# Performance work log

Hardware: AMD Instinct MI355X
Metric: run time of the kernel (lower is better)

The kernel has to match this reference:

```python
import jax, jax.numpy as jnp
import numpy as np

D_MODEL = 512
N_HEADS = 8
N_KV_HEADS = 2
HEAD_DIM = 64
PITCH_VOCAB = 128


def setup_inputs() -> dict:
    key = jax.random.key(0)
    ks = jax.random.split(key, 6)
    B, T, P = 2, 256, 12
    s = lambda fan_in: 1.0 / np.sqrt(fan_in)
    hidden_states = jax.random.normal(ks[0], (B, T, P, D_MODEL), dtype=jnp.float32)
    Wq = jax.random.normal(ks[1], (D_MODEL, N_HEADS * HEAD_DIM), dtype=jnp.float32) * s(D_MODEL)
    Wk = jax.random.normal(ks[2], (D_MODEL, N_KV_HEADS * HEAD_DIM), dtype=jnp.float32) * s(D_MODEL)
    Wv = jax.random.normal(ks[3], (D_MODEL, N_KV_HEADS * HEAD_DIM), dtype=jnp.float32) * s(D_MODEL)
    Wo = jax.random.normal(ks[4], (N_HEADS * HEAD_DIM, D_MODEL), dtype=jnp.float32) * s(N_HEADS * HEAD_DIM)
    pitch_table = jax.random.normal(ks[5], (PITCH_VOCAB, HEAD_DIM), dtype=jnp.float32)
    return {"hidden_states": hidden_states, "Wq": Wq, "Wk": Wk, "Wv": Wv, "Wo": Wo, "pitch_table": pitch_table}


def reference(hidden_states, Wq, Wk, Wv, Wo, pitch_table):
    B, T, P, C = hidden_states.shape
    H, Hkv, d = N_HEADS, N_KV_HEADS, HEAD_DIM
    rep = H // Hkv

    q = (hidden_states @ Wq).reshape(B, T, P, H, d)
    k = (hidden_states @ Wk).reshape(B, T, P, Hkv, d)
    v = (hidden_states @ Wv).reshape(B, T, P, Hkv, d)

    # GQA repeat_kv: (B,T,P,Hkv,d) -> (B,T,P,H,d)
    k = jnp.repeat(k, rep, axis=3)
    v = jnp.repeat(v, rep, axis=3)

    # additive pitch bias on q and k
    pitch_emb = pitch_table[jnp.arange(P)]  # (P, d)
    bias = pitch_emb[None, None, :, None, :]
    q = q + bias
    k = k + bias

    # flatten (T,P) -> S and move heads forward: (B,H,S,d)
    S = T * P
    q = q.transpose(0, 3, 1, 2, 4).reshape(B, H, S, d)
    k = k.transpose(0, 3, 1, 2, 4).reshape(B, H, S, d)
    v = v.transpose(0, 3, 1, 2, 4).reshape(B, H, S, d)

    scale = 1.0 / jnp.sqrt(jnp.asarray(d, dtype=q.dtype))
    attn = jax.nn.softmax(jnp.einsum('bhqd,bhkd->bhqk', q, k) * scale, axis=-1)
    out = jnp.einsum('bhqk,bhkd->bhqd', attn, v)  # (B,H,S,d)

    out = out.reshape(B, H, T, P, d).transpose(0, 2, 3, 1, 4).reshape(B, T, P, H * d)
    return out @ Wo
```

## Files before the change

kernel.cpp:

```cpp
#include <hip/hip_runtime.h>
#include <hip/hip_fp16.h>

#define B_   2
#define T_   256
#define P_   12
#define C_   512
#define H_   8
#define HKV_ 2
#define D_   64
#define S_   (T_ * P_)
#define M_   (B_ * S_)
#define NQKV 768
#define KSPLIT 2
#define KHALF (S_ / KSPLIT)

typedef _Float16 half8_t __attribute__((ext_vector_type(8)));
typedef _Float16 half4_t __attribute__((ext_vector_type(4)));
typedef _Float16 half2_t __attribute__((ext_vector_type(2)));
typedef float    float4_t __attribute__((ext_vector_type(4)));

#if __has_builtin(__builtin_amdgcn_exp2f)
#define EXP2(x) __builtin_amdgcn_exp2f(x)
#else
#define EXP2(x) __expf((x) * 0.69314718f)
#endif

static __device__ inline half2_t pack_h2(float a, float b) {
#if __has_builtin(__builtin_amdgcn_cvt_pkrtz)
    return __builtin_bit_cast(half2_t, __builtin_amdgcn_cvt_pkrtz(a, b));
#else
    half2_t r; r[0] = (_Float16)a; r[1] = (_Float16)b; return r;
#endif
}

#define SOFT_SHIFT 20.0f
#define SOFT_CLAMP 35.5f
#define QSCALE (0.125f * 1.44269504f)

__global__ __launch_bounds__(256) void prep_kernel(
    const float* __restrict__ hs,
    const float* __restrict__ Wq, const float* __restrict__ Wk,
    const float* __restrict__ Wv, const float* __restrict__ Wo,
    _Float16* __restrict__ hs16,
    _Float16* __restrict__ wcatT,
    _Float16* __restrict__ woT)
{
    const int blk = blockIdx.x;
    const int tid = threadIdx.x;

    if (blk < 160) {
        __shared__ __attribute__((aligned(16))) _Float16 Ts[64][72];
        const float* src; int srcN, col0; _Float16* dst; int n0, k0;
        if (blk < 96) {
            int nt = blk / 8, kt = blk % 8;
            n0 = nt * 64; k0 = kt * 64; dst = wcatT;
            if (n0 < 512)      { src = Wq; srcN = 512; col0 = n0; }
            else if (n0 < 640) { src = Wk; srcN = 128; col0 = n0 - 512; }
            else               { src = Wv; srcN = 128; col0 = n0 - 640; }
        } else {
            int t = blk - 96;
            int nt = t / 8, kt = t % 8;
            n0 = nt * 64; k0 = kt * 64; dst = woT;
            src = Wo; srcN = 512; col0 = n0;
        }
#pragma unroll
        for (int i = 0; i < 4; ++i) {
            int row = i * 16 + (tid >> 4);
            int cg  = tid & 15;
            float4_t v = *(const float4_t*)(src + (size_t)(k0 + row) * srcN + col0 + cg * 4);
            Ts[cg * 4 + 0][row] = (_Float16)v[0];
            Ts[cg * 4 + 1][row] = (_Float16)v[1];
            Ts[cg * 4 + 2][row] = (_Float16)v[2];
            Ts[cg * 4 + 3][row] = (_Float16)v[3];
        }
        __syncthreads();
#pragma unroll
        for (int i = 0; i < 2; ++i) {
            int seg = i * 256 + tid;
            int row = seg >> 3, s = seg & 7;
            *(half8_t*)(dst + (size_t)(n0 + row) * 512 + k0 + s * 8) =
                *(const half8_t*)&Ts[row][s * 8];
        }
    } else {
        int base = (blk - 160) * 4096;
#pragma unroll
        for (int i = 0; i < 16; ++i) {
            int f4 = base + i * 256 + tid;
            float4_t v = *(const float4_t*)(hs + (size_t)f4 * 4);
            half4_t hv;
            hv[0] = (_Float16)v[0]; hv[1] = (_Float16)v[1];
            hv[2] = (_Float16)v[2]; hv[3] = (_Float16)v[3];
            *(half4_t*)(hs16 + (size_t)f4 * 4) = hv;
        }
    }
}

__global__ __launch_bounds__(256) void qkv_kernel(
    const _Float16* __restrict__ A,
    const _Float16* __restrict__ WT,
    const float* __restrict__ pitch,
    _Float16* __restrict__ qb,
    _Float16* __restrict__ kb,
    _Float16* __restrict__ vb)
{
    const int m0   = blockIdx.x * 64;
    const int n0   = blockIdx.y * 128;
    const int tid  = threadIdx.x;
    const int wv   = tid >> 6;
    const int lane = tid & 63;
    const int ln   = lane & 15;
    const int quad = lane >> 4;
    const int wm   = (wv & 1) * 32;
    const int wn   = (wv >> 1) * 64;

    __shared__ __attribute__((aligned(16))) _Float16 As[64][72];
    __shared__ __attribute__((aligned(16))) _Float16 Bs[128][72];

    float4_t acc[2][4];
#pragma unroll
    for (int ms = 0; ms < 2; ++ms)
#pragma unroll
        for (int nt = 0; nt < 4; ++nt) acc[ms][nt] = (float4_t){0.f, 0.f, 0.f, 0.f};

    const int srow = tid >> 3;
    const int ss   = tid & 7;

    half8_t ar[2], br[4];
#pragma unroll
    for (int i = 0; i < 2; ++i)
        ar[i] = *(const half8_t*)&A[(size_t)(m0 + i * 32 + srow) * 512 + ss * 8];
#pragma unroll
    for (int i = 0; i < 4; ++i)
        br[i] = *(const half8_t*)&WT[(size_t)(n0 + i * 32 + srow) * 512 + ss * 8];

    for (int k0 = 0; k0 < 512; k0 += 64) {
        __syncthreads();
#pragma unroll
        for (int i = 0; i < 2; ++i) *(half8_t*)&As[i * 32 + srow][ss * 8] = ar[i];
#pragma unroll
        for (int i = 0; i < 4; ++i) *(half8_t*)&Bs[i * 32 + srow][ss * 8] = br[i];
        __syncthreads();

        if (k0 + 64 < 512) {
#pragma unroll
            for (int i = 0; i < 2; ++i)
                ar[i] = *(const half8_t*)&A[(size_t)(m0 + i * 32 + srow) * 512 + k0 + 64 + ss * 8];
#pragma unroll
            for (int i = 0; i < 4; ++i)
                br[i] = *(const half8_t*)&WT[(size_t)(n0 + i * 32 + srow) * 512 + k0 + 64 + ss * 8];
        }

#pragma unroll
        for (int ks = 0; ks < 2; ++ks) {
            half8_t af[2];
#pragma unroll
            for (int ms = 0; ms < 2; ++ms)
                af[ms] = *(const half8_t*)&As[wm + ms * 16 + ln][ks * 32 + quad * 8];
#pragma unroll
            for (int nt = 0; nt < 4; ++nt) {
                half8_t bf = *(const half8_t*)&Bs[wn + nt * 16 + ln][ks * 32 + quad * 8];
#pragma unroll
                for (int ms = 0; ms < 2; ++ms)
                    acc[ms][nt] = __builtin_amdgcn_mfma_f32_16x16x32_f16(af[ms], bf, acc[ms][nt], 0, 0, 0);
            }
        }
    }

    const int region = (n0 < 512) ? 0 : (n0 < 640 ? 1 : 2);
#pragma unroll
    for (int ms = 0; ms < 2; ++ms) {
#pragma unroll
        for (int nt = 0; nt < 4; ++nt) {
            int n = n0 + wn + nt * 16 + ln;
#pragma unroll
            for (int r = 0; r < 4; ++r) {
                int m = m0 + wm + ms * 16 + quad * 4 + r;
                int b = m / S_;
                int s = m - b * S_;
                int p = s % P_;
                float v = acc[ms][nt][r];
                if (region == 0) {
                    int h = n >> 6, dd = n & 63;
                    v = (v + pitch[p * 64 + dd]) * QSCALE;
                    qb[(((size_t)(b * H_ + h)) * S_ + s) * 64 + dd] = (_Float16)v;
                } else if (region == 1) {
                    int nn = n - 512, h = nn >> 6, dd = nn & 63;
                    v = v + pitch[p * 64 + dd];
                    kb[(((size_t)(b * HKV_ + h)) * S_ + s) * 64 + dd] = (_Float16)v;
                } else {
                    int nn = n - 640, h = nn >> 6, dd = nn & 63;
                    vb[(((size_t)(b * HKV_ + h)) * 64 + dd) * S_ + s] = (_Float16)v;
                }
            }
        }
    }
}

__global__ __launch_bounds__(256) void attn_kernel(
    const _Float16* __restrict__ qbuf,
    const _Float16* __restrict__ kbuf,
    const _Float16* __restrict__ vtb,
    _Float16* __restrict__ opA,
    _Float16* __restrict__ opB,
    float* __restrict__ lpA,
    float* __restrict__ lpB)
{
    const int qblk = blockIdx.x;
    const int bh   = blockIdx.y;
    const int kz   = blockIdx.z;
    const int bb   = bh >> 3;
    const int h    = bh & 7;
    const int hkv  = h >> 2;
    const int tid  = threadIdx.x;
    const int w    = tid >> 6;
    const int lane = tid & 63;
    const int ln   = lane & 15;
    const int quad = lane >> 4;

    _Float16* op = kz ? opB : opA;
    float*    lp = kz ? lpB : lpA;

    const _Float16* Q  = qbuf + ((size_t)(bb * H_ + h)) * S_ * 64;
    const _Float16* K  = kbuf + ((size_t)(bb * HKV_ + hkv)) * S_ * 64;
    const _Float16* Vt = vtb  + ((size_t)(bb * HKV_ + hkv)) * 64 * S_;

    __shared__ __attribute__((aligned(16))) _Float16 Ks[64][80];
    __shared__ __attribute__((aligned(16))) _Float16 VT[64][80];
    __shared__ __attribute__((aligned(16))) _Float16 Ps[4][32][40];

    const int qbase = qblk * 64 + (w & 1) * 32;
    const int kk0   = (w >> 1) * 32;
    const int ktlo  = kz * KHALF;

    half8_t qfrag[2][2];
#pragma unroll
    for (int sub = 0; sub < 2; ++sub)
#pragma unroll
        for (int ks = 0; ks < 2; ++ks)
            qfrag[sub][ks] = *(const half8_t*)&Q[(size_t)(qbase + sub * 16 + ln) * 64 + ks * 32 + quad * 8];

    float4_t o[2][4];
#pragma unroll
    for (int sub = 0; sub < 2; ++sub)
#pragma unroll
        for (int nt = 0; nt < 4; ++nt) o[sub][nt] = (float4_t){0.f, 0.f, 0.f, 0.f};
    float lr[2][4] = {{0.f,0.f,0.f,0.f},{0.f,0.f,0.f,0.f}};

    const int j0 = tid >> 3, s0 = tid & 7;
    const int j1 = j0 + 32;
    const int r0 = ((j0 & 1) << 4) | ((j0 >> 5) << 5) | ((j0 >> 1) & 15);
    const int r1 = ((j1 & 1) << 4) | ((j1 >> 5) << 5) | ((j1 >> 1) & 15);

    half8_t kr0, kr1, vr0, vr1;
    kr0 = *(const half8_t*)&K[(size_t)(ktlo + j0) * 64 + s0 * 8];
    kr1 = *(const half8_t*)&K[(size_t)(ktlo + j1) * 64 + s0 * 8];
    vr0 = *(const half8_t*)&Vt[(size_t)j0 * S_ + ktlo + s0 * 8];
    vr1 = *(const half8_t*)&Vt[(size_t)j1 * S_ + ktlo + s0 * 8];

    for (int kt = ktlo; kt < ktlo + KHALF; kt += 64) {
        __syncthreads();
        *(half8_t*)&Ks[r0][s0 * 8] = kr0;
        *(half8_t*)&Ks[r1][s0 * 8] = kr1;
        *(half8_t*)&VT[j0][s0 * 8] = vr0;
        *(half8_t*)&VT[j1][s0 * 8] = vr1;
        __syncthreads();

        if (kt + 64 < ktlo + KHALF) {
            kr0 = *(const half8_t*)&K[(size_t)(kt + 64 + j0) * 64 + s0 * 8];
            kr1 = *(const half8_t*)&K[(size_t)(kt + 64 + j1) * 64 + s0 * 8];
            vr0 = *(const half8_t*)&Vt[(size_t)j0 * S_ + kt + 64 + s0 * 8];
            vr1 = *(const half8_t*)&Vt[(size_t)j1 * S_ + kt + 64 + s0 * 8];
        }

        float4_t sf[2][2];
#pragma unroll
        for (int c = 0; c < 2; ++c) {
            sf[c][0] = (float4_t){0.f, 0.f, 0.f, 0.f};
            sf[c][1] = (float4_t){0.f, 0.f, 0.f, 0.f};
#pragma unroll
            for (int ks = 0; ks < 2; ++ks) {
                half8_t kf = *(const half8_t*)&Ks[kk0 + c * 16 + ln][ks * 32 + quad * 8];
                sf[c][0] = __builtin_amdgcn_mfma_f32_16x16x32_f16(qfrag[0][ks], kf, sf[c][0], 0, 0, 0);
                sf[c][1] = __builtin_amdgcn_mfma_f32_16x16x32_f16(qfrag[1][ks], kf, sf[c][1], 0, 0, 0);
            }
        }

#pragma unroll
        for (int sub = 0; sub < 2; ++sub) {
#pragma unroll
            for (int r = 0; r < 4; ++r) {
                float p0 = EXP2(fminf(sf[0][sub][r], SOFT_CLAMP) - SOFT_SHIFT);
                float p1 = EXP2(fminf(sf[1][sub][r], SOFT_CLAMP) - SOFT_SHIFT);
                lr[sub][r] += p0 + p1;
                *(half2_t*)&Ps[w][sub * 16 + quad * 4 + r][2 * ln] = pack_h2(p0, p1);
            }
        }

        half8_t pf0 = *(const half8_t*)&Ps[w][ln][quad * 8];
        half8_t pf1 = *(const half8_t*)&Ps[w][16 + ln][quad * 8];
#pragma unroll
        for (int nt = 0; nt < 4; ++nt) {
            half8_t vf = *(const half8_t*)&VT[nt * 16 + ln][kk0 + quad * 8];
            o[0][nt] = __builtin_amdgcn_mfma_f32_16x16x32_f16(pf0, vf, o[0][nt], 0, 0, 0);
            o[1][nt] = __builtin_amdgcn_mfma_f32_16x16x32_f16(pf1, vf, o[1][nt], 0, 0, 0);
        }
    }

    __syncthreads();
    if (w >= 2) {
        float* od = (w == 2) ? (float*)&Ks[0][0] : (float*)&VT[0][0];
#pragma unroll
        for (int sub = 0; sub < 2; ++sub)
#pragma unroll
            for (int nt = 0; nt < 4; ++nt)
                *(float4_t*)&od[lane * 32 + (sub * 4 + nt) * 4] = o[sub][nt];
        float* ld = (float*)&Ps[0][0][0] + (w - 2) * 512;
#pragma unroll
        for (int sub = 0; sub < 2; ++sub)
#pragma unroll
            for (int r = 0; r < 4; ++r)
                ld[lane * 8 + sub * 4 + r] = lr[sub][r];
    }
    __syncthreads();
    if (w < 2) {
        const float* os = (w == 0) ? (const float*)&Ks[0][0] : (const float*)&VT[0][0];
        const float* ls = (const float*)&Ps[0][0][0] + w * 512;
#pragma unroll
        for (int sub = 0; sub < 2; ++sub) {
#pragma unroll
            for (int r = 0; r < 4; ++r) {
                float l = lr[sub][r] + ls[lane * 8 + sub * 4 + r];
                l += __shfl_xor(l, 1);
                l += __shfl_xor(l, 2);
                l += __shfl_xor(l, 4);
                l += __shfl_xor(l, 8);
                float inv = 1.0f / l;
                int qg = qbase + sub * 16 + quad * 4 + r;
                size_t base = ((size_t)(bb * S_ + qg)) * 512 + h * 64;
#pragma unroll
                for (int nt = 0; nt < 4; ++nt) {
                    float vsum = o[sub][nt][r] + os[lane * 32 + (sub * 4 + nt) * 4 + r];
                    op[base + nt * 16 + ln] = (_Float16)(vsum * inv);
                }
                if (ln == 0)
                    lp[(size_t)(bb * H_ + h) * S_ + qg] = l;
            }
        }
    }
}

__global__ __launch_bounds__(256) void combine_kernel(
    _Float16* __restrict__ opA,
    const _Float16* __restrict__ opB,
    const float* __restrict__ lpA,
    const float* __restrict__ lpB)
{
    int i = blockIdx.x * 256 + threadIdx.x;
    int base = i * 8;
    int bs  = base >> 9;
    int col = base & 511;
    int h   = col >> 6;
    int b   = (bs >= S_) ? 1 : 0;
    int q   = bs - b * S_;
    size_t row = (size_t)(b * H_ + h) * S_ + q;
    float la = lpA[row], lb = lpB[row];
    float s  = la + lb;
    float wa = la / s, wb = lb / s;
    half8_t a8 = *(const half8_t*)(opA + (size_t)base);
    half8_t b8 = *(const half8_t*)(opB + (size_t)base);
    half8_t o8;
#pragma unroll
    for (int j = 0; j < 8; ++j)
        o8[j] = (_Float16)((float)a8[j] * wa + (float)b8[j] * wb);
    *(half8_t*)(opA + (size_t)base) = o8;
}

__global__ __launch_bounds__(256) void proj_out_kernel(
    const _Float16* __restrict__ A,
    const _Float16* __restrict__ WT,
    float* __restrict__ outp)
{
    const int m0   = blockIdx.x * 64;
    const int n0   = blockIdx.y * 128;
    const int tid  = threadIdx.x;
    const int wv   = tid >> 6;
    const int lane = tid & 63;
    const int ln   = lane & 15;
    const int quad = lane >> 4;
    const int wm   = (wv & 1) * 32;
    const int wn   = (wv >> 1) * 64;

    __shared__ __attribute__((aligned(16))) _Float16 As[64][72];
    __shared__ __attribute__((aligned(16))) _Float16 Bs[128][72];

    float4_t acc[2][4];
#pragma unroll
    for (int ms = 0; ms < 2; ++ms)
#pragma unroll
        for (int nt = 0; nt < 4; ++nt) acc[ms][nt] = (float4_t){0.f, 0.f, 0.f, 0.f};

    const int srow = tid >> 3;
    const int ss   = tid & 7;

    half8_t ar[2], br[4];
#pragma unroll
    for (int i = 0; i < 2; ++i)
        ar[i] = *(const half8_t*)&A[(size_t)(m0 + i * 32 + srow) * 512 + ss * 8];
#pragma unroll
    for (int i = 0; i < 4; ++i)
        br[i] = *(const half8_t*)&WT[(size_t)(n0 + i * 32 + srow) * 512 + ss * 8];

    for (int k0 = 0; k0 < 512; k0 += 64) {
        __syncthreads();
#pragma unroll
        for (int i = 0; i < 2; ++i) *(half8_t*)&As[i * 32 + srow][ss * 8] = ar[i];
#pragma unroll
        for (int i = 0; i < 4; ++i) *(half8_t*)&Bs[i * 32 + srow][ss * 8] = br[i];
        __syncthreads();

        if (k0 + 64 < 512) {
#pragma unroll
            for (int i = 0; i < 2; ++i)
                ar[i] = *(const half8_t*)&A[(size_t)(m0 + i * 32 + srow) * 512 + k0 + 64 + ss * 8];
#pragma unroll
            for (int i = 0; i < 4; ++i)
                br[i] = *(const half8_t*)&WT[(size_t)(n0 + i * 32 + srow) * 512 + k0 + 64 + ss * 8];
        }

#pragma unroll
        for (int ks = 0; ks < 2; ++ks) {
            half8_t af[2];
#pragma unroll
            for (int ms = 0; ms < 2; ++ms)
                af[ms] = *(const half8_t*)&As[wm + ms * 16 + ln][ks * 32 + quad * 8];
#pragma unroll
            for (int nt = 0; nt < 4; ++nt) {
                half8_t bf = *(const half8_t*)&Bs[wn + nt * 16 + ln][ks * 32 + quad * 8];
#pragma unroll
                for (int ms = 0; ms < 2; ++ms)
                    acc[ms][nt] = __builtin_amdgcn_mfma_f32_16x16x32_f16(af[ms], bf, acc[ms][nt], 0, 0, 0);
            }
        }
    }

#pragma unroll
    for (int ms = 0; ms < 2; ++ms) {
#pragma unroll
        for (int nt = 0; nt < 4; ++nt) {
            int n = n0 + wn + nt * 16 + ln;
#pragma unroll
            for (int r = 0; r < 4; ++r) {
                int m = m0 + wm + ms * 16 + quad * 4 + r;
                outp[(size_t)m * 512 + n] = acc[ms][nt][r];
            }
        }
    }
}

extern "C" void kernel_launch(void* const* d_in, const int* in_sizes, int n_in,
                              void* d_out, int out_size, void* d_ws, size_t ws_size,
                              hipStream_t stream) {
    const float* hs    = (const float*)d_in[0];
    const float* Wq    = (const float*)d_in[1];
    const float* Wk    = (const float*)d_in[2];
    const float* Wv    = (const float*)d_in[3];
    const float* Wo    = (const float*)d_in[4];
    const float* pitch = (const float*)d_in[5];
    float* out = (float*)d_out;

    _Float16* hs16  = (_Float16*)d_ws;
    _Float16* opA   = hs16;
    _Float16* q_buf = hs16 + (size_t)M_ * 512;
    _Float16* k_buf = q_buf + (size_t)B_ * H_ * S_ * 64;
    _Float16* v_buf = k_buf + (size_t)B_ * HKV_ * S_ * 64;
    _Float16* wcatT = v_buf + (size_t)B_ * HKV_ * S_ * 64;
    _Float16* woT   = wcatT + (size_t)NQKV * 512;
    _Float16* opB   = woT   + (size_t)512 * 512;
    float*    lpA   = (float*)(opB + (size_t)M_ * 512);
    float*    lpB   = lpA + (size_t)B_ * H_ * S_;

    prep_kernel<<<352, 256, 0, stream>>>(hs, Wq, Wk, Wv, Wo, hs16, wcatT, woT);
    qkv_kernel<<<dim3(M_ / 64, NQKV / 128), 256, 0, stream>>>(hs16, wcatT, pitch, q_buf, k_buf, v_buf);
    attn_kernel<<<dim3(S_ / 64, B_ * H_, KSPLIT), 256, 0, stream>>>(q_buf, k_buf, v_buf, opA, opB, lpA, lpB);
    combine_kernel<<<(M_ * 512 / 8) / 256, 256, 0, stream>>>(opA, opB, lpA, lpB);
    proj_out_kernel<<<dim3(M_ / 64, 4), 256, 0, stream>>>(opA, woT, out);
}
```

Measured before the change: 181.5 us.

## Enlarge attention tile to 128 queries with 512 threads and fold softmax shift

The attention kernel now runs 8 waves per block covering 128 query rows, so each K/V tile staged in shared memory is reused by twice as many queries. Each thread loads only one K and one V vector per tile. The softmax shift is folded into the MFMA accumulator initial value, and the row sum now uses a packed fp16 dot2 on the packed probabilities. Row-sum reductions move before the cross-wave combine, and the scratch buffers are laid out as an LDS union. The risks are fewer blocks in flight, heavier register and LDS use per block, and fp16 rounding in the row sum.

```diff
diff --git a/kernel.cpp b/kernel.cpp
--- a/kernel.cpp
+++ b/kernel.cpp
@@ -17,6 +17,7 @@
 typedef _Float16 half8_t __attribute__((ext_vector_type(8)));
 typedef _Float16 half4_t __attribute__((ext_vector_type(4)));
 typedef _Float16 half2_t __attribute__((ext_vector_type(2)));
+typedef __fp16   raw2_t  __attribute__((ext_vector_type(2)));
 typedef float    float4_t __attribute__((ext_vector_type(4)));
 
 #if __has_builtin(__builtin_amdgcn_exp2f)
@@ -25,16 +26,8 @@
 #define EXP2(x) __expf((x) * 0.69314718f)
 #endif
 
-static __device__ inline half2_t pack_h2(float a, float b) {
-#if __has_builtin(__builtin_amdgcn_cvt_pkrtz)
-    return __builtin_bit_cast(half2_t, __builtin_amdgcn_cvt_pkrtz(a, b));
-#else
-    half2_t r; r[0] = (_Float16)a; r[1] = (_Float16)b; return r;
-#endif
-}
-
 #define SOFT_SHIFT 20.0f
-#define SOFT_CLAMP 35.5f
+#define SOFT_CLAMP2 15.5f
 #define QSCALE (0.125f * 1.44269504f)
 
 __global__ __launch_bounds__(256) void prep_kernel(
@@ -196,7 +189,7 @@
     }
 }
 
-__global__ __launch_bounds__(256) void attn_kernel(
+__global__ __launch_bounds__(512) void attn_kernel(
     const _Float16* __restrict__ qbuf,
     const _Float16* __restrict__ kbuf,
     const _Float16* __restrict__ vtb,
@@ -224,12 +217,17 @@
     const _Float16* K  = kbuf + ((size_t)(bb * HKV_ + hkv)) * S_ * 64;
     const _Float16* Vt = vtb  + ((size_t)(bb * HKV_ + hkv)) * 64 * S_;
 
-    __shared__ __attribute__((aligned(16))) _Float16 Ks[64][80];
-    __shared__ __attribute__((aligned(16))) _Float16 VT[64][80];
-    __shared__ __attribute__((aligned(16))) _Float16 Ps[4][32][40];
-
-    const int qbase = qblk * 64 + (w & 1) * 32;
-    const int kk0   = (w >> 1) * 32;
+    __shared__ __attribute__((aligned(16))) union LdsU {
+        struct Main {
+            _Float16 Ks[64][72];
+            _Float16 VT[64][72];
+            _Float16 Ps[8][32][40];
+        } m;
+        float pool[9728];
+    } lds;
+
+    const int qbase = qblk * 128 + (w & 3) * 32;
+    const int kk0   = (w >> 2) * 32;
     const int ktlo  = kz * KHALF;
 
     half8_t qfrag[2][2];
@@ -247,39 +245,35 @@
     float lr[2][4] = {{0.f,0.f,0.f,0.f},{0.f,0.f,0.f,0.f}};
 
     const int j0 = tid >> 3, s0 = tid & 7;
-    const int j1 = j0 + 32;
     const int r0 = ((j0 & 1) << 4) | ((j0 >> 5) << 5) | ((j0 >> 1) & 15);
-    const int r1 = ((j1 & 1) << 4) | ((j1 >> 5) << 5) | ((j1 >> 1) & 15);
-
-    half8_t kr0, kr1, vr0, vr1;
+
+    half8_t kr0, vr0;
     kr0 = *(const half8_t*)&K[(size_t)(ktlo + j0) * 64 + s0 * 8];
-    kr1 = *(const half8_t*)&K[(size_t)(ktlo + j1) * 64 + s0 * 8];
     vr0 = *(const half8_t*)&Vt[(size_t)j0 * S_ + ktlo + s0 * 8];
-    vr1 = *(const half8_t*)&Vt[(size_t)j1 * S_ + ktlo + s0 * 8];
+
+#if __has_builtin(__builtin_amdgcn_fdot2)
+    const raw2_t one2 = {(__fp16)1.0f, (__fp16)1.0f};
+#endif
 
     for (int kt = ktlo; kt < ktlo + KHALF; kt += 64) {
         __syncthreads();
-        *(half8_t*)&Ks[r0][s0 * 8] = kr0;
-        *(half8_t*)&Ks[r1][s0 * 8] = kr1;
-        *(half8_t*)&VT[j0][s0 * 8] = vr0;
-        *(half8_t*)&VT[j1][s0 * 8] = vr1;
+        *(half8_t*)&lds.m.Ks[r0][s0 * 8] = kr0;
+        *(half8_t*)&lds.m.VT[j0][s0 * 8] = vr0;
         __syncthreads();
 
         if (kt + 64 < ktlo + KHALF) {
             kr0 = *(const half8_t*)&K[(size_t)(kt + 64 + j0) * 64 + s0 * 8];
-            kr1 = *(const half8_t*)&K[(size_t)(kt + 64 + j1) * 64 + s0 * 8];
             vr0 = *(const half8_t*)&Vt[(size_t)j0 * S_ + kt + 64 + s0 * 8];
-            vr1 = *(const half8_t*)&Vt[(size_t)j1 * S_ + kt + 64 + s0 * 8];
         }
 
         float4_t sf[2][2];
 #pragma unroll
         for (int c = 0; c < 2; ++c) {
-            sf[c][0] = (float4_t){0.f, 0.f, 0.f, 0.f};
-            sf[c][1] = (float4_t){0.f, 0.f, 0.f, 0.f};
+            sf[c][0] = (float4_t){-SOFT_SHIFT, -SOFT_SHIFT, -SOFT_SHIFT, -SOFT_SHIFT};
+            sf[c][1] = (float4_t){-SOFT_SHIFT, -SOFT_SHIFT, -SOFT_SHIFT, -SOFT_SHIFT};
 #pragma unroll
             for (int ks = 0; ks < 2; ++ks) {
-                half8_t kf = *(const half8_t*)&Ks[kk0 + c * 16 + ln][ks * 32 + quad * 8];
+                half8_t kf = *(const half8_t*)&lds.m.Ks[kk0 + c * 16 + ln][ks * 32 + quad * 8];
                 sf[c][0] = __builtin_amdgcn_mfma_f32_16x16x32_f16(qfrag[0][ks], kf, sf[c][0], 0, 0, 0);
                 sf[c][1] = __builtin_amdgcn_mfma_f32_16x16x32_f16(qfrag[1][ks], kf, sf[c][1], 0, 0, 0);
             }
@@ -289,57 +283,73 @@
         for (int sub = 0; sub < 2; ++sub) {
 #pragma unroll
             for (int r = 0; r < 4; ++r) {
-                float p0 = EXP2(fminf(sf[0][sub][r], SOFT_CLAMP) - SOFT_SHIFT);
-                float p1 = EXP2(fminf(sf[1][sub][r], SOFT_CLAMP) - SOFT_SHIFT);
+                float p0 = EXP2(fminf(sf[0][sub][r], SOFT_CLAMP2));
+                float p1 = EXP2(fminf(sf[1][sub][r], SOFT_CLAMP2));
+#if __has_builtin(__builtin_amdgcn_cvt_pkrtz)
+                raw2_t pk = __builtin_amdgcn_cvt_pkrtz(p0, p1);
+#else
+                raw2_t pk = {(__fp16)p0, (__fp16)p1};
+#endif
+#if __has_builtin(__builtin_amdgcn_fdot2)
+                lr[sub][r] = __builtin_amdgcn_fdot2(pk, one2, lr[sub][r], false);
+#else
                 lr[sub][r] += p0 + p1;
-                *(half2_t*)&Ps[w][sub * 16 + quad * 4 + r][2 * ln] = pack_h2(p0, p1);
-            }
-        }
-
-        half8_t pf0 = *(const half8_t*)&Ps[w][ln][quad * 8];
-        half8_t pf1 = *(const half8_t*)&Ps[w][16 + ln][quad * 8];
+#endif
+                *(raw2_t*)&lds.m.Ps[w][sub * 16 + quad * 4 + r][2 * ln] = pk;
+            }
+        }
+
+        half8_t pf0 = *(const half8_t*)&lds.m.Ps[w][ln][quad * 8];
+        half8_t pf1 = *(const half8_t*)&lds.m.Ps[w][16 + ln][quad * 8];
 #pragma unroll
         for (int nt = 0; nt < 4; ++nt) {
-            half8_t vf = *(const half8_t*)&VT[nt * 16 + ln][kk0 + quad * 8];
+            half8_t vf = *(const half8_t*)&lds.m.VT[nt * 16 + ln][kk0 + quad * 8];
             o[0][nt] = __builtin_amdgcn_mfma_f32_16x16x32_f16(pf0, vf, o[0][nt], 0, 0, 0);
             o[1][nt] = __builtin_amdgcn_mfma_f32_16x16x32_f16(pf1, vf, o[1][nt], 0, 0, 0);
         }
     }
 
+#pragma unroll
+    for (int sub = 0; sub < 2; ++sub)
+#pragma unroll
+        for (int r = 0; r < 4; ++r) {
+            float l = lr[sub][r];
+            l += __shfl_xor(l, 1);
+            l += __shfl_xor(l, 2);
+            l += __shfl_xor(l, 4);
+            l += __shfl_xor(l, 8);
+            lr[sub][r] = l;
+        }
+
     __syncthreads();
-    if (w >= 2) {
-        float* od = (w == 2) ? (float*)&Ks[0][0] : (float*)&VT[0][0];
-#pragma unroll
-        for (int sub = 0; sub < 2; ++sub)
+    if (w >= 4) {
+        float* bf = lds.pool + (w - 4) * 2080;
+#pragma unroll
+        for (int sub = 0; sub < 2; ++sub) {
 #pragma unroll
             for (int nt = 0; nt < 4; ++nt)
-                *(float4_t*)&od[lane * 32 + (sub * 4 + nt) * 4] = o[sub][nt];
-        float* ld = (float*)&Ps[0][0][0] + (w - 2) * 512;
-#pragma unroll
-        for (int sub = 0; sub < 2; ++sub)
-#pragma unroll
-            for (int r = 0; r < 4; ++r)
-                ld[lane * 8 + sub * 4 + r] = lr[sub][r];
+                *(float4_t*)&bf[lane * 32 + (sub * 4 + nt) * 4] = o[sub][nt];
+            if (ln == 0) {
+                float4_t lv = {lr[sub][0], lr[sub][1], lr[sub][2], lr[sub][3]};
+                *(float4_t*)&bf[2048 + sub * 16 + quad * 4] = lv;
+            }
+        }
     }
     __syncthreads();
-    if (w < 2) {
-        const float* os = (w == 0) ? (const float*)&Ks[0][0] : (const float*)&VT[0][0];
-        const float* ls = (const float*)&Ps[0][0][0] + w * 512;
+    if (w < 4) {
+        const float* bf = lds.pool + w * 2080;
 #pragma unroll
         for (int sub = 0; sub < 2; ++sub) {
+            float4_t lv = *(const float4_t*)&bf[2048 + sub * 16 + quad * 4];
 #pragma unroll
             for (int r = 0; r < 4; ++r) {
-                float l = lr[sub][r] + ls[lane * 8 + sub * 4 + r];
-                l += __shfl_xor(l, 1);
-                l += __shfl_xor(l, 2);
-                l += __shfl_xor(l, 4);
-                l += __shfl_xor(l, 8);
+                float l = lr[sub][r] + lv[r];
                 float inv = 1.0f / l;
                 int qg = qbase + sub * 16 + quad * 4 + r;
                 size_t base = ((size_t)(bb * S_ + qg)) * 512 + h * 64;
 #pragma unroll
                 for (int nt = 0; nt < 4; ++nt) {
-                    float vsum = o[sub][nt][r] + os[lane * 32 + (sub * 4 + nt) * 4 + r];
+                    float vsum = o[sub][nt][r] + bf[lane * 32 + (sub * 4 + nt) * 4 + r];
                     op[base + nt * 16 + ln] = (_Float16)(vsum * inv);
                 }
                 if (ln == 0)
@@ -481,7 +491,7 @@
 
     prep_kernel<<<352, 256, 0, stream>>>(hs, Wq, Wk, Wv, Wo, hs16, wcatT, woT);
     qkv_kernel<<<dim3(M_ / 64, NQKV / 128), 256, 0, stream>>>(hs16, wcatT, pitch, q_buf, k_buf, v_buf);
-    attn_kernel<<<dim3(S_ / 64, B_ * H_, KSPLIT), 256, 0, stream>>>(q_buf, k_buf, v_buf, opA, opB, lpA, lpB);
+    attn_kernel<<<dim3(S_ / 128, B_ * H_, KSPLIT), 512, 0, stream>>>(q_buf, k_buf, v_buf, opA, opB, lpA, lpB);
     combine_kernel<<<(M_ * 512 / 8) / 256, 256, 0, stream>>>(opA, opB, lpA, lpB);
     proj_out_kernel<<<dim3(M_ / 64, 4), 256, 0, stream>>>(opA, woT, out);
 }
```

After: 170.5 us. 1.06x faster.
